# Optimization experiments

Hardware: AMD Instinct MI355X
Metric: run time of the kernel (lower is better)

## Reference

```python
import jax, jax.numpy as jnp
import numpy as np

MIN_NORM = 1e-15
N = 10000        # num_nodes
E = 320000       # num edges (avg degree 32)
F_IN = 512       # in_features
HID = 256        # hardcoded encoder hidden dim
D_HYP = 2        # Poincare embedding dim
HEIGHT = 2
MAX_SIZE = 0.999
MIN_SCALE = HEIGHT * (MAX_SIZE / (HEIGHT + 1))  # = 0.666, scale clamp lower bound
MAX_SCALE = MAX_SIZE


def setup_inputs() -> dict:
    key = jax.random.key(0)
    ks = jax.random.split(key, 5)
    feature = jax.random.normal(ks[0], (N, F_IN), jnp.float32)
    edge_index = jax.random.randint(ks[1], (2, E), 0, N, dtype=jnp.int64)
    W1 = jax.random.normal(ks[2], (F_IN, HID), jnp.float32) / np.sqrt(F_IN).astype(np.float32)
    b1 = jnp.zeros((HID,), jnp.float32)
    W2 = jax.random.normal(ks[3], (HID, D_HYP), jnp.float32) / np.sqrt(HID).astype(np.float32)
    b2 = jnp.zeros((D_HYP,), jnp.float32)
    scale = jnp.ones((1,), jnp.float32)  # init_size overridden to 1.0 in __init__
    return {"feature": feature, "edge_index": edge_index, "W1": W1, "b1": b1,
            "W2": W2, "b2": b2, "scale": scale}


def _gcn_agg(h, src, dst):
    # symmetric-normalized edge_index gather/aggregate (message passing)
    deg = jax.ops.segment_sum(jnp.ones((src.shape[0],), h.dtype), dst, num_segments=N)
    deg = jnp.maximum(deg, 1.0)
    norm = jax.lax.rsqrt(deg[src] * deg[dst])            # [E]
    msg = h[src] * norm[:, None]                          # [E, C] gather (irregular)
    return jax.ops.segment_sum(msg, dst, num_segments=N)  # [N, C] scatter-add


def reference(feature, edge_index, W1, b1, W2, b2, scale):
    src, dst = edge_index[0], edge_index[1]
    # 2-layer graph encoder (linear -> aggregate -> relu, linear -> aggregate)
    h = jax.nn.relu(_gcn_agg(feature @ W1 + b1, src, dst))   # [N, HID]
    u = _gcn_agg(h @ W2 + b2, src, dst)                      # [N, D_HYP] tangent at origin
    # lift to Lorentz model (k=-1) via expmap0: x = [cosh|u|, sinh|u| * u/|u|]
    un = jnp.maximum(jnp.linalg.norm(u, axis=-1, keepdims=True), MIN_NORM)
    x_l = jnp.concatenate([jnp.cosh(un), jnp.sinh(un) * u / un], axis=-1)  # [N, D_HYP+1]
    # Lorentz -> Poincare: p = x_space / (1 + x_time)
    p = x_l[:, 1:] / (1.0 + x_l[:, :1])
    # normalize: F.normalize(p, dim=-1) * scale.clamp(min_size, max_size)
    pn = jnp.maximum(jnp.linalg.norm(p, axis=-1, keepdims=True), 1e-12)
    s = jnp.clip(scale, MIN_SCALE, MAX_SCALE)
    p = p / pn * s
    # project onto Poincare ball of curvature k=-1 with eps=MIN_NORM
    norm = jnp.maximum(jnp.linalg.norm(p, axis=-1, keepdims=True), MIN_NORM)
    maxnorm = 1.0 - MIN_NORM
    return jnp.where(norm > maxnorm, p / norm * maxnorm, p)
```

## Files before the change

### kernel.cpp

```cpp
#include <hip/hip_runtime.h>
#include <math.h>

#define N_NODES 10000
#define N_EDGES 320000
#define F_IN 512
#define HID 256
#define PAD_DEG 80
#define LDSTR 40
#define N_TILES (157 * 4)

typedef _Float16 half8 __attribute__((ext_vector_type(8)));
typedef float floatx4 __attribute__((ext_vector_type(4)));

__device__ __forceinline__ void fma4(float4& acc, float s, const float4& v) {
    acc.x += s * v.x; acc.y += s * v.y; acc.z += s * v.z; acc.w += s * v.w;
}


__global__ void k_build(const int* __restrict__ ei, const float* __restrict__ W1,
                        int* __restrict__ count, int* __restrict__ csr,
                        _Float16* __restrict__ Bt_hi, _Float16* __restrict__ Bt_lo) {
    int i = blockIdx.x * blockDim.x + threadIdx.x;
    if (i < F_IN * HID) {
        int k = i >> 8, n = i & 255;
        float v = W1[i];
        _Float16 hi = (_Float16)v;
        Bt_hi[n * F_IN + k] = hi;
        Bt_lo[n * F_IN + k] = (_Float16)(v - (float)hi);
    }
    if (i < N_EDGES) {
        int src = ei[i];
        int dst = ei[N_EDGES + i];
        int pos = atomicAdd(&count[dst], 1);
        csr[dst * PAD_DEG + pos] = src;
    }
}


__global__ __launch_bounds__(256) void k_gemm(const float* __restrict__ A,
                                              const _Float16* __restrict__ Bt_hi,
                                              const _Float16* __restrict__ Bt_lo,
                                              const float* __restrict__ b1,
                                              float* __restrict__ h0) {
    __shared__ _Float16 As_hi[64 * LDSTR], As_lo[64 * LDSTR];
    __shared__ _Float16 Bs_hi[64 * LDSTR], Bs_lo[64 * LDSTR];
    const int tid = threadIdx.x;
    const int lane = tid & 63, w = tid >> 6;
    const int wm = (w >> 1) * 32, wn = (w & 1) * 32;
    const int quad = lane >> 4, l15 = lane & 15;
    const int r = tid >> 2, c = (tid & 3) << 3;
    const int t = blockIdx.x;
    const int row0 = (t >> 2) * 64, col0 = (t & 3) * 64;
    floatx4 acc[2][2] = {};

    for (int k0 = 0; k0 < F_IN; k0 += 32) {
        float av[8];
        int arow = row0 + r;
        if (arow < N_NODES) {
            float4 v0 = *(const float4*)(A + (size_t)arow * F_IN + k0 + c);
            float4 v1 = *(const float4*)(A + (size_t)arow * F_IN + k0 + c + 4);
            av[0] = v0.x; av[1] = v0.y; av[2] = v0.z; av[3] = v0.w;
            av[4] = v1.x; av[5] = v1.y; av[6] = v1.z; av[7] = v1.w;
        } else {
            #pragma unroll
            for (int i = 0; i < 8; ++i) av[i] = 0.f;
        }
        half8 hhi, hlo;
        #pragma unroll
        for (int i = 0; i < 8; ++i) {
            _Float16 h = (_Float16)av[i];
            hhi[i] = h;
            hlo[i] = (_Float16)(av[i] - (float)h);
        }
        *(half8*)&As_hi[r * LDSTR + c] = hhi;
        *(half8*)&As_lo[r * LDSTR + c] = hlo;
        *(half8*)&Bs_hi[r * LDSTR + c] = *(const half8*)(Bt_hi + (size_t)(col0 + r) * F_IN + k0 + c);
        *(half8*)&Bs_lo[r * LDSTR + c] = *(const half8*)(Bt_lo + (size_t)(col0 + r) * F_IN + k0 + c);
        __syncthreads();
        half8 a_hi[2], a_lo[2], b_hi[2], b_lo[2];
        #pragma unroll
        for (int mi = 0; mi < 2; ++mi) {
            int mr = wm + mi * 16 + l15;
            a_hi[mi] = *(half8*)&As_hi[mr * LDSTR + quad * 8];
            a_lo[mi] = *(half8*)&As_lo[mr * LDSTR + quad * 8];
        }
        #pragma unroll
        for (int ni = 0; ni < 2; ++ni) {
            int nr = wn + ni * 16 + l15;
            b_hi[ni] = *(half8*)&Bs_hi[nr * LDSTR + quad * 8];
            b_lo[ni] = *(half8*)&Bs_lo[nr * LDSTR + quad * 8];
        }
        #pragma unroll
        for (int mi = 0; mi < 2; ++mi)
            #pragma unroll
            for (int ni = 0; ni < 2; ++ni) {
                acc[mi][ni] = __builtin_amdgcn_mfma_f32_16x16x32_f16(a_hi[mi], b_hi[ni], acc[mi][ni], 0, 0, 0);
                acc[mi][ni] = __builtin_amdgcn_mfma_f32_16x16x32_f16(a_hi[mi], b_lo[ni], acc[mi][ni], 0, 0, 0);
                acc[mi][ni] = __builtin_amdgcn_mfma_f32_16x16x32_f16(a_lo[mi], b_hi[ni], acc[mi][ni], 0, 0, 0);
            }
        __syncthreads();
    }
    #pragma unroll
    for (int mi = 0; mi < 2; ++mi)
        #pragma unroll
        for (int ni = 0; ni < 2; ++ni) {
            int colb = col0 + wn + ni * 16 + l15;
            float bias = b1[colb];
            #pragma unroll
            for (int reg = 0; reg < 4; ++reg) {
                int rowb = row0 + wm + mi * 16 + quad * 4 + reg;
                if (rowb < N_NODES) h0[(size_t)rowb * HID + colb] = acc[mi][ni][reg] + bias;
            }
        }
}


__global__ __launch_bounds__(256) void k_agg1(const float* __restrict__ h0,
                                              const int* __restrict__ csr,
                                              const int* __restrict__ count,
                                              const float* __restrict__ W2,
                                              const float* __restrict__ b2,
                                              float* __restrict__ u0) {
    int n = blockIdx.x * 4 + (threadIdx.x >> 6);
    int lane = threadIdx.x & 63;
    if (n >= N_NODES) return;
    int deg = count[n];
    float degd = (float)(deg > 0 ? deg : 1);
    const int* row = csr + (size_t)n * PAD_DEG;
    int off = lane << 2;
    float4 acc0 = {0,0,0,0}, acc1 = {0,0,0,0}, acc2 = {0,0,0,0}, acc3 = {0,0,0,0};
    int j = 0;
    for (; j + 8 <= deg; j += 8) {
        int s0 = row[j+0], s1 = row[j+1], s2 = row[j+2], s3 = row[j+3];
        int s4 = row[j+4], s5 = row[j+5], s6 = row[j+6], s7 = row[j+7];
        int c0 = count[s0], c1 = count[s1], c2 = count[s2], c3 = count[s3];
        int c4 = count[s4], c5 = count[s5], c6 = count[s6], c7 = count[s7];
        float4 v0 = *(const float4*)(h0 + (size_t)s0 * HID + off);
        float4 v1 = *(const float4*)(h0 + (size_t)s1 * HID + off);
        float4 v2 = *(const float4*)(h0 + (size_t)s2 * HID + off);
        float4 v3 = *(const float4*)(h0 + (size_t)s3 * HID + off);
        float4 v4 = *(const float4*)(h0 + (size_t)s4 * HID + off);
        float4 v5 = *(const float4*)(h0 + (size_t)s5 * HID + off);
        float4 v6 = *(const float4*)(h0 + (size_t)s6 * HID + off);
        float4 v7 = *(const float4*)(h0 + (size_t)s7 * HID + off);
        fma4(acc0, rsqrtf((float)(c0 > 0 ? c0 : 1) * degd), v0);
        fma4(acc1, rsqrtf((float)(c1 > 0 ? c1 : 1) * degd), v1);
        fma4(acc2, rsqrtf((float)(c2 > 0 ? c2 : 1) * degd), v2);
        fma4(acc3, rsqrtf((float)(c3 > 0 ? c3 : 1) * degd), v3);
        fma4(acc0, rsqrtf((float)(c4 > 0 ? c4 : 1) * degd), v4);
        fma4(acc1, rsqrtf((float)(c5 > 0 ? c5 : 1) * degd), v5);
        fma4(acc2, rsqrtf((float)(c6 > 0 ? c6 : 1) * degd), v6);
        fma4(acc3, rsqrtf((float)(c7 > 0 ? c7 : 1) * degd), v7);
    }
    for (; j < deg; ++j) {
        int s = row[j];
        int cs = count[s];
        float4 v = *(const float4*)(h0 + (size_t)s * HID + off);
        fma4(acc0, rsqrtf((float)(cs > 0 ? cs : 1) * degd), v);
    }
    acc0.x += acc1.x + acc2.x + acc3.x;
    acc0.y += acc1.y + acc2.y + acc3.y;
    acc0.z += acc1.z + acc2.z + acc3.z;
    acc0.w += acc1.w + acc2.w + acc3.w;
    acc0.x = fmaxf(acc0.x, 0.f); acc0.y = fmaxf(acc0.y, 0.f);
    acc0.z = fmaxf(acc0.z, 0.f); acc0.w = fmaxf(acc0.w, 0.f);
    float4 wa = *(const float4*)(W2 + (lane << 3));
    float4 wb = *(const float4*)(W2 + (lane << 3) + 4);
    float p0 = acc0.x * wa.x + acc0.y * wa.z + acc0.z * wb.x + acc0.w * wb.z;
    float p1 = acc0.x * wa.y + acc0.y * wa.w + acc0.z * wb.y + acc0.w * wb.w;
    #pragma unroll
    for (int o = 32; o > 0; o >>= 1) {
        p0 += __shfl_down(p0, o);
        p1 += __shfl_down(p1, o);
    }
    if (lane == 0) {
        u0[2 * n]     = p0 + b2[0];
        u0[2 * n + 1] = p1 + b2[1];
    }
}


__global__ __launch_bounds__(256) void k_agg2(const float* __restrict__ u0,
                                              const int* __restrict__ csr,
                                              const int* __restrict__ count,
                                              const float* __restrict__ scale,
                                              float* __restrict__ out) {
    int n = blockIdx.x * 4 + (threadIdx.x >> 6);
    int lane = threadIdx.x & 63;
    if (n >= N_NODES) return;
    int deg = count[n];
    float degd = (float)(deg > 0 ? deg : 1);
    const int* row = csr + (size_t)n * PAD_DEG;
    float a0 = 0.f, a1 = 0.f;
    for (int j = lane; j < deg; j += 64) {
        int s = row[j];
        int cs = count[s];
        float wq = rsqrtf((float)(cs > 0 ? cs : 1) * degd);
        float2 uv = *(const float2*)(u0 + 2 * (size_t)s);
        a0 += wq * uv.x;
        a1 += wq * uv.y;
    }
    #pragma unroll
    for (int o = 32; o > 0; o >>= 1) {
        a0 += __shfl_down(a0, o);
        a1 += __shfl_down(a1, o);
    }
    if (lane == 0) {
        float un = fmaxf(sqrtf(a0 * a0 + a1 * a1), 1e-15f);
        float t = tanhf(0.5f * un) / un;
        float p0 = a0 * t, p1 = a1 * t;
        float pn = fmaxf(sqrtf(p0 * p0 + p1 * p1), 1e-12f);
        float s = fminf(fmaxf(scale[0], 0.666f), 0.999f);
        p0 = p0 / pn * s; p1 = p1 / pn * s;
        float nn = fmaxf(sqrtf(p0 * p0 + p1 * p1), 1e-15f);
        if (nn > 1.0f) { p0 = p0 / nn; p1 = p1 / nn; }
        out[2 * n]     = p0;
        out[2 * n + 1] = p1;
    }
}


extern "C" void kernel_launch(void* const* d_in, const int* in_sizes, int n_in,
                              void* d_out, int out_size, void* d_ws, size_t ws_size,
                              hipStream_t stream) {
    const float* feature = (const float*)d_in[0];
    const int*   ei      = (const int*)d_in[1];
    const float* W1      = (const float*)d_in[2];
    const float* b1      = (const float*)d_in[3];
    const float* W2      = (const float*)d_in[4];
    const float* b2      = (const float*)d_in[5];
    const float* scale   = (const float*)d_in[6];
    float* out = (float*)d_out;

    char* W = (char*)d_ws;
    int*      count = (int*)W;
    int*      csr   = (int*)(W + 40960);
    float*    h0    = (float*)(W + 3240960);
    float*    u0    = (float*)(W + 13480960);
    _Float16* Bt_hi = (_Float16*)(W + 13560960);
    _Float16* Bt_lo = (_Float16*)(W + 13823104);

    (void)hipMemsetAsync(count, 0, 10240 * sizeof(int), stream);

    k_build<<<dim3((N_EDGES + 255) / 256), dim3(256), 0, stream>>>(
        ei, W1, count, csr, Bt_hi, Bt_lo);
    k_gemm<<<dim3(N_TILES), dim3(256), 0, stream>>>(feature, Bt_hi, Bt_lo, b1, h0);
    k_agg1<<<dim3((N_NODES + 3) / 4), dim3(256), 0, stream>>>(h0, csr, count, W2, b2, u0);
    k_agg2<<<dim3((N_NODES + 3) / 4), dim3(256), 0, stream>>>(u0, csr, count, scale, out);
}
```

Measured before the change: 158.9 us.

## Split layer-1 aggregation across channel quarters and read GEMM B operand directly

The first aggregation kernel now runs a 2D grid, with each wave handling 64 channels of one node instead of all 256 as float4 per lane. It writes four partial W2 projections per node, which the second aggregation sums together with the bias. The aim is more waves in flight for the latency-bound gather, at the cost of scalar loads, four-fold redundant CSR and count reads, and an extra partial buffer. Separately, the GEMM drops the LDS staging of B and loads B fragments straight from global memory, which cuts LDS traffic but relies on cache hits for reuse.

```diff
diff --git a/kernel.cpp b/kernel.cpp
--- a/kernel.cpp
+++ b/kernel.cpp
@@ -11,10 +11,6 @@
 
 typedef _Float16 half8 __attribute__((ext_vector_type(8)));
 typedef float floatx4 __attribute__((ext_vector_type(4)));
-
-__device__ __forceinline__ void fma4(float4& acc, float s, const float4& v) {
-    acc.x += s * v.x; acc.y += s * v.y; acc.z += s * v.z; acc.w += s * v.w;
-}
 
 
 __global__ void k_build(const int* __restrict__ ei, const float* __restrict__ W1,
@@ -43,7 +39,6 @@
                                               const float* __restrict__ b1,
                                               float* __restrict__ h0) {
     __shared__ _Float16 As_hi[64 * LDSTR], As_lo[64 * LDSTR];
-    __shared__ _Float16 Bs_hi[64 * LDSTR], Bs_lo[64 * LDSTR];
     const int tid = threadIdx.x;
     const int lane = tid & 63, w = tid >> 6;
     const int wm = (w >> 1) * 32, wn = (w & 1) * 32;
@@ -74,8 +69,6 @@
         }
         *(half8*)&As_hi[r * LDSTR + c] = hhi;
         *(half8*)&As_lo[r * LDSTR + c] = hlo;
-        *(half8*)&Bs_hi[r * LDSTR + c] = *(const half8*)(Bt_hi + (size_t)(col0 + r) * F_IN + k0 + c);
-        *(half8*)&Bs_lo[r * LDSTR + c] = *(const half8*)(Bt_lo + (size_t)(col0 + r) * F_IN + k0 + c);
         __syncthreads();
         half8 a_hi[2], a_lo[2], b_hi[2], b_lo[2];
         #pragma unroll
@@ -86,9 +79,9 @@
         }
         #pragma unroll
         for (int ni = 0; ni < 2; ++ni) {
-            int nr = wn + ni * 16 + l15;
-            b_hi[ni] = *(half8*)&Bs_hi[nr * LDSTR + quad * 8];
-            b_lo[ni] = *(half8*)&Bs_lo[nr * LDSTR + quad * 8];
+            size_t boff = (size_t)(col0 + wn + ni * 16 + l15) * F_IN + k0 + quad * 8;
+            b_hi[ni] = *(const half8*)(Bt_hi + boff);
+            b_lo[ni] = *(const half8*)(Bt_lo + boff);
         }
         #pragma unroll
         for (int mi = 0; mi < 2; ++mi)
@@ -119,70 +112,59 @@
                                               const int* __restrict__ csr,
                                               const int* __restrict__ count,
                                               const float* __restrict__ W2,
-                                              const float* __restrict__ b2,
-                                              float* __restrict__ u0) {
+                                              float* __restrict__ u0p) {
     int n = blockIdx.x * 4 + (threadIdx.x >> 6);
     int lane = threadIdx.x & 63;
-    if (n >= N_NODES) return;
+    int p = blockIdx.y;
     int deg = count[n];
     float degd = (float)(deg > 0 ? deg : 1);
     const int* row = csr + (size_t)n * PAD_DEG;
-    int off = lane << 2;
-    float4 acc0 = {0,0,0,0}, acc1 = {0,0,0,0}, acc2 = {0,0,0,0}, acc3 = {0,0,0,0};
+    const int ch = (p << 6) + lane;
+    const float* hcol = h0 + ch;
+    float acc0 = 0.f, acc1 = 0.f, acc2 = 0.f, acc3 = 0.f;
     int j = 0;
     for (; j + 8 <= deg; j += 8) {
         int s0 = row[j+0], s1 = row[j+1], s2 = row[j+2], s3 = row[j+3];
         int s4 = row[j+4], s5 = row[j+5], s6 = row[j+6], s7 = row[j+7];
         int c0 = count[s0], c1 = count[s1], c2 = count[s2], c3 = count[s3];
         int c4 = count[s4], c5 = count[s5], c6 = count[s6], c7 = count[s7];
-        float4 v0 = *(const float4*)(h0 + (size_t)s0 * HID + off);
-        float4 v1 = *(const float4*)(h0 + (size_t)s1 * HID + off);
-        float4 v2 = *(const float4*)(h0 + (size_t)s2 * HID + off);
-        float4 v3 = *(const float4*)(h0 + (size_t)s3 * HID + off);
-        float4 v4 = *(const float4*)(h0 + (size_t)s4 * HID + off);
-        float4 v5 = *(const float4*)(h0 + (size_t)s5 * HID + off);
-        float4 v6 = *(const float4*)(h0 + (size_t)s6 * HID + off);
-        float4 v7 = *(const float4*)(h0 + (size_t)s7 * HID + off);
-        fma4(acc0, rsqrtf((float)(c0 > 0 ? c0 : 1) * degd), v0);
-        fma4(acc1, rsqrtf((float)(c1 > 0 ? c1 : 1) * degd), v1);
-        fma4(acc2, rsqrtf((float)(c2 > 0 ? c2 : 1) * degd), v2);
-        fma4(acc3, rsqrtf((float)(c3 > 0 ? c3 : 1) * degd), v3);
-        fma4(acc0, rsqrtf((float)(c4 > 0 ? c4 : 1) * degd), v4);
-        fma4(acc1, rsqrtf((float)(c5 > 0 ? c5 : 1) * degd), v5);
-        fma4(acc2, rsqrtf((float)(c6 > 0 ? c6 : 1) * degd), v6);
-        fma4(acc3, rsqrtf((float)(c7 > 0 ? c7 : 1) * degd), v7);
+        float v0 = hcol[(size_t)s0 * HID], v1 = hcol[(size_t)s1 * HID];
+        float v2 = hcol[(size_t)s2 * HID], v3 = hcol[(size_t)s3 * HID];
+        float v4 = hcol[(size_t)s4 * HID], v5 = hcol[(size_t)s5 * HID];
+        float v6 = hcol[(size_t)s6 * HID], v7 = hcol[(size_t)s7 * HID];
+        acc0 += rsqrtf((float)(c0 > 0 ? c0 : 1) * degd) * v0;
+        acc1 += rsqrtf((float)(c1 > 0 ? c1 : 1) * degd) * v1;
+        acc2 += rsqrtf((float)(c2 > 0 ? c2 : 1) * degd) * v2;
+        acc3 += rsqrtf((float)(c3 > 0 ? c3 : 1) * degd) * v3;
+        acc0 += rsqrtf((float)(c4 > 0 ? c4 : 1) * degd) * v4;
+        acc1 += rsqrtf((float)(c5 > 0 ? c5 : 1) * degd) * v5;
+        acc2 += rsqrtf((float)(c6 > 0 ? c6 : 1) * degd) * v6;
+        acc3 += rsqrtf((float)(c7 > 0 ? c7 : 1) * degd) * v7;
     }
     for (; j < deg; ++j) {
         int s = row[j];
         int cs = count[s];
-        float4 v = *(const float4*)(h0 + (size_t)s * HID + off);
-        fma4(acc0, rsqrtf((float)(cs > 0 ? cs : 1) * degd), v);
-    }
-    acc0.x += acc1.x + acc2.x + acc3.x;
-    acc0.y += acc1.y + acc2.y + acc3.y;
-    acc0.z += acc1.z + acc2.z + acc3.z;
-    acc0.w += acc1.w + acc2.w + acc3.w;
-    acc0.x = fmaxf(acc0.x, 0.f); acc0.y = fmaxf(acc0.y, 0.f);
-    acc0.z = fmaxf(acc0.z, 0.f); acc0.w = fmaxf(acc0.w, 0.f);
-    float4 wa = *(const float4*)(W2 + (lane << 3));
-    float4 wb = *(const float4*)(W2 + (lane << 3) + 4);
-    float p0 = acc0.x * wa.x + acc0.y * wa.z + acc0.z * wb.x + acc0.w * wb.z;
-    float p1 = acc0.x * wa.y + acc0.y * wa.w + acc0.z * wb.y + acc0.w * wb.w;
+        acc0 += rsqrtf((float)(cs > 0 ? cs : 1) * degd) * hcol[(size_t)s * HID];
+    }
+    float a = fmaxf(acc0 + acc1 + acc2 + acc3, 0.f);
+    float p0 = a * W2[2 * ch];
+    float p1 = a * W2[2 * ch + 1];
     #pragma unroll
     for (int o = 32; o > 0; o >>= 1) {
         p0 += __shfl_down(p0, o);
         p1 += __shfl_down(p1, o);
     }
     if (lane == 0) {
-        u0[2 * n]     = p0 + b2[0];
-        u0[2 * n + 1] = p1 + b2[1];
-    }
-}
-
-
-__global__ __launch_bounds__(256) void k_agg2(const float* __restrict__ u0,
+        u0p[(size_t)n * 8 + p * 2]     = p0;
+        u0p[(size_t)n * 8 + p * 2 + 1] = p1;
+    }
+}
+
+
+__global__ __launch_bounds__(256) void k_agg2(const float* __restrict__ u0p,
                                               const int* __restrict__ csr,
                                               const int* __restrict__ count,
+                                              const float* __restrict__ b2,
                                               const float* __restrict__ scale,
                                               float* __restrict__ out) {
     int n = blockIdx.x * 4 + (threadIdx.x >> 6);
@@ -191,14 +173,16 @@
     int deg = count[n];
     float degd = (float)(deg > 0 ? deg : 1);
     const int* row = csr + (size_t)n * PAD_DEG;
+    float b20 = b2[0], b21 = b2[1];
     float a0 = 0.f, a1 = 0.f;
     for (int j = lane; j < deg; j += 64) {
         int s = row[j];
         int cs = count[s];
         float wq = rsqrtf((float)(cs > 0 ? cs : 1) * degd);
-        float2 uv = *(const float2*)(u0 + 2 * (size_t)s);
-        a0 += wq * uv.x;
-        a1 += wq * uv.y;
+        float4 qa = *(const float4*)(u0p + (size_t)s * 8);
+        float4 qb = *(const float4*)(u0p + (size_t)s * 8 + 4);
+        a0 += wq * (qa.x + qa.z + qb.x + qb.z + b20);
+        a1 += wq * (qa.y + qa.w + qb.y + qb.w + b21);
     }
     #pragma unroll
     for (int o = 32; o > 0; o >>= 1) {
@@ -236,15 +220,15 @@
     int*      count = (int*)W;
     int*      csr   = (int*)(W + 40960);
     float*    h0    = (float*)(W + 3240960);
-    float*    u0    = (float*)(W + 13480960);
-    _Float16* Bt_hi = (_Float16*)(W + 13560960);
-    _Float16* Bt_lo = (_Float16*)(W + 13823104);
+    float*    u0p   = (float*)(W + 13480960);
+    _Float16* Bt_hi = (_Float16*)(W + 14760960);
+    _Float16* Bt_lo = (_Float16*)(W + 15023104);
 
     (void)hipMemsetAsync(count, 0, 10240 * sizeof(int), stream);
 
     k_build<<<dim3((N_EDGES + 255) / 256), dim3(256), 0, stream>>>(
         ei, W1, count, csr, Bt_hi, Bt_lo);
     k_gemm<<<dim3(N_TILES), dim3(256), 0, stream>>>(feature, Bt_hi, Bt_lo, b1, h0);
-    k_agg1<<<dim3((N_NODES + 3) / 4), dim3(256), 0, stream>>>(h0, csr, count, W2, b2, u0);
-    k_agg2<<<dim3((N_NODES + 3) / 4), dim3(256), 0, stream>>>(u0, csr, count, scale, out);
-}
+    k_agg1<<<dim3(2500, 4), dim3(256), 0, stream>>>(h0, csr, count, W2, u0p);
+    k_agg2<<<dim3(2500), dim3(256), 0, stream>>>(u0p, csr, count, b2, scale, out);
+}
```

New measurement: 179.3 us. 1.13x slower.

## Merge CSR build into GEMM launch and fold count zeroing into W1 split

Applied to the files above, without the earlier changes.

The separate memset is removed by zeroing the degree counts inside a small W1-split kernel (k_pre). Edge-to-CSR construction now runs as extra blocks appended to the GEMM grid, so the atomic scatter overlaps with the matrix multiply. Two launches replace three stream operations and the small CSR build can hide behind GEMM tiles. In exchange the CSR blocks compete with GEMM tiles for CUs, and GEMM blocks now depend on k_pre having finished the W1 split first.

```diff
diff --git a/kernel.cpp b/kernel.cpp
--- a/kernel.cpp
+++ b/kernel.cpp
@@ -8,6 +8,7 @@
 #define PAD_DEG 80
 #define LDSTR 40
 #define N_TILES (157 * 4)
+#define BUILD_BLKS ((N_EDGES + 255) / 256)
 
 typedef _Float16 half8 __attribute__((ext_vector_type(8)));
 typedef float floatx4 __attribute__((ext_vector_type(4)));
@@ -17,34 +18,43 @@
 }
 
 
-__global__ void k_build(const int* __restrict__ ei, const float* __restrict__ W1,
-                        int* __restrict__ count, int* __restrict__ csr,
-                        _Float16* __restrict__ Bt_hi, _Float16* __restrict__ Bt_lo) {
+__global__ __launch_bounds__(256) void k_pre(const float* __restrict__ W1,
+                                             int* __restrict__ count,
+                                             _Float16* __restrict__ Bt_hi,
+                                             _Float16* __restrict__ Bt_lo) {
     int i = blockIdx.x * blockDim.x + threadIdx.x;
-    if (i < F_IN * HID) {
-        int k = i >> 8, n = i & 255;
-        float v = W1[i];
-        _Float16 hi = (_Float16)v;
-        Bt_hi[n * F_IN + k] = hi;
-        Bt_lo[n * F_IN + k] = (_Float16)(v - (float)hi);
-    }
-    if (i < N_EDGES) {
-        int src = ei[i];
-        int dst = ei[N_EDGES + i];
-        int pos = atomicAdd(&count[dst], 1);
-        csr[dst * PAD_DEG + pos] = src;
-    }
-}
-
-
-__global__ __launch_bounds__(256) void k_gemm(const float* __restrict__ A,
-                                              const _Float16* __restrict__ Bt_hi,
-                                              const _Float16* __restrict__ Bt_lo,
-                                              const float* __restrict__ b1,
-                                              float* __restrict__ h0) {
+    if (i < 10240) count[i] = 0;
+    int k = i >> 8, n = i & 255;
+    float v = W1[i];
+    _Float16 hi = (_Float16)v;
+    Bt_hi[n * F_IN + k] = hi;
+    Bt_lo[n * F_IN + k] = (_Float16)(v - (float)hi);
+}
+
+
+__global__ __launch_bounds__(256) void k_combo(const float* __restrict__ A,
+                                               const _Float16* __restrict__ Bt_hi,
+                                               const _Float16* __restrict__ Bt_lo,
+                                               const float* __restrict__ b1,
+                                               float* __restrict__ h0,
+                                               const int* __restrict__ ei,
+                                               int* __restrict__ count,
+                                               int* __restrict__ csr) {
     __shared__ _Float16 As_hi[64 * LDSTR], As_lo[64 * LDSTR];
     __shared__ _Float16 Bs_hi[64 * LDSTR], Bs_lo[64 * LDSTR];
     const int tid = threadIdx.x;
+
+    if (blockIdx.x >= N_TILES) {
+        int e = (blockIdx.x - N_TILES) * 256 + tid;
+        if (e < N_EDGES) {
+            int src = ei[e];
+            int dst = ei[N_EDGES + e];
+            int pos = atomicAdd(&count[dst], 1);
+            csr[dst * PAD_DEG + pos] = src;
+        }
+        return;
+    }
+
     const int lane = tid & 63, w = tid >> 6;
     const int wm = (w >> 1) * 32, wn = (w & 1) * 32;
     const int quad = lane >> 4, l15 = lane & 15;
@@ -240,11 +250,9 @@
     _Float16* Bt_hi = (_Float16*)(W + 13560960);
     _Float16* Bt_lo = (_Float16*)(W + 13823104);
 
-    (void)hipMemsetAsync(count, 0, 10240 * sizeof(int), stream);
-
-    k_build<<<dim3((N_EDGES + 255) / 256), dim3(256), 0, stream>>>(
-        ei, W1, count, csr, Bt_hi, Bt_lo);
-    k_gemm<<<dim3(N_TILES), dim3(256), 0, stream>>>(feature, Bt_hi, Bt_lo, b1, h0);
+    k_pre<<<dim3(512), dim3(256), 0, stream>>>(W1, count, Bt_hi, Bt_lo);
+    k_combo<<<dim3(N_TILES + BUILD_BLKS), dim3(256), 0, stream>>>(
+        feature, Bt_hi, Bt_lo, b1, h0, ei, count, csr);
     k_agg1<<<dim3((N_NODES + 3) / 4), dim3(256), 0, stream>>>(h0, csr, count, W2, b2, u0);
     k_agg2<<<dim3((N_NODES + 3) / 4), dim3(256), 0, stream>>>(u0, csr, count, scale, out);
 }
```

Measured after the change: 153.7 us. 1.03x faster.
